# Performance work log

Hardware: AMD Instinct MI355X
Metric: run time of the kernel (lower is better)

The kernel has to match this reference:

```python
import jax, jax.numpy as jnp
import numpy as np

R = 64
N = 7

_D_PARMS = [[1], [0, 1], [8, 1, 1], [16, 25, 3, 1], [260, 153, 65, 6, 1],
            [1856, 21, 629, 137, 10, 1], [26240, 26603, 11253, 1990, 263, 15, 1]]

def _get_variance(n, r):
    res = 0.0
    for i, x in enumerate(_D_PARMS[n - 1]):
        x = float(x)
        for j in range(i):
            x *= (r - j)
        res += x
    return res

_DECAYS = [1.0] + [float(np.sqrt(_get_variance(i + 1, R) / _get_variance(i, R)))
                   for i in range(1, N)]
_DECAY_CUMSUM = float(np.sqrt(N))


def setup_inputs() -> dict:
    key = jax.random.key(0)
    M = jax.random.normal(key, (8192, R * R), dtype=jnp.float32)
    return {"M": M}


def reference(M) -> jnp.ndarray:
    shape = M.shape[:-1]
    Mm = M.reshape(shape + (R, R))            # [..., r, r]
    # power series: cumsum = sum_i (M^(i+1)) / prod(decays[:i+1]) (decays[0]=1)
    P = Mm
    acc = Mm
    for i in range(1, N):                     # fixed N=7 unrolled chain
        P = jnp.matmul(P, Mm) / _DECAYS[i]
        acc = acc + P
    # NOTE: the torch code's cumsum[..., mask, mask].zero_() operates on a copy
    # (advanced indexing), so it is a no-op on cumsum; we faithfully omit it.
    acc = acc / _DECAY_CUMSUM
    return acc.reshape(shape + (R * R,))
```

## Files before the change

### kernel.cpp

```cpp
#include <hip/hip_runtime.h>
#include <hip/hip_bf16.h>
#include <math.h>


#define RDIM 64
#define LDSP 72

using bf16x8 = __attribute__((ext_vector_type(8))) short;
using f32x4  = __attribute__((ext_vector_type(4))) float;

__device__ __forceinline__ short f2bf(float x) {
    __hip_bfloat16 h = __float2bfloat16(x);
    union { __hip_bfloat16 b; short s; } u; u.b = h; return u.s;
}
__device__ __forceinline__ float bf2f(short s) {
    union { short s; __hip_bfloat16 b; } u; u.s = s;
    return __bfloat162float(u.b);
}

__global__ __launch_bounds__(256) void power_series_kernel(
        const float* __restrict__ M, float* __restrict__ out) {
    __shared__ short PAhi[RDIM][LDSP];
    __shared__ short PAlo[RDIM][LDSP];
    __shared__ short MThi[RDIM][LDSP];
    __shared__ short MTlo[RDIM][LDSP];

    const int tid  = threadIdx.x;
    const int lane = tid & 63;
    const int wave = tid >> 6;
    const int l15  = lane & 15;
    const int quad = lane >> 4;

    const float* Mg = M   + (size_t)blockIdx.x * (RDIM * RDIM);
    float*       Og = out + (size_t)blockIdx.x * (RDIM * RDIM);

    {
        const float4* Mg4 = reinterpret_cast<const float4*>(Mg);
        #pragma unroll
        for (int v = 0; v < 4; ++v) {
            float4 x = Mg4[tid + 256 * v];
            int e0  = (tid + 256 * v) * 4;
            int row = e0 >> 6;
            int col = e0 & 63;
            float xs[4] = {x.x, x.y, x.z, x.w};
            short hs[4], ls[4];
            #pragma unroll
            for (int j = 0; j < 4; ++j) {
                short h = f2bf(xs[j]);
                hs[j] = h;
                ls[j] = f2bf(xs[j] - bf2f(h));
            }
            short4 hv; hv.x = hs[0]; hv.y = hs[1]; hv.z = hs[2]; hv.w = hs[3];
            short4 lv; lv.x = ls[0]; lv.y = ls[1]; lv.z = ls[2]; lv.w = ls[3];
            *reinterpret_cast<short4*>(&PAhi[row][col]) = hv;
            *reinterpret_cast<short4*>(&PAlo[row][col]) = lv;
            #pragma unroll
            for (int j = 0; j < 4; ++j) {
                MThi[col + j][row] = hs[j];
                MTlo[col + j][row] = ls[j];
            }
        }
    }
    __syncthreads();

    bf16x8 bhi[4][2], blo[4][2];
    #pragma unroll
    for (int t = 0; t < 4; ++t) {
        #pragma unroll
        for (int kb = 0; kb < 2; ++kb) {
            int n = t * 16 + l15;
            int k = kb * 32 + quad * 8;
            bhi[t][kb] = *reinterpret_cast<const bf16x8*>(&MThi[n][k]);
            blo[t][kb] = *reinterpret_cast<const bf16x8*>(&MTlo[n][k]);
        }
    }

    const double V[7] = {1.0, 64.0, 4104.0, 263696.0, 17021060.0,
                         1104218816.0, 72260728960.0};
    float invd[7];
    invd[0] = 1.0f;
    #pragma unroll
    for (int i = 1; i < 7; ++i) invd[i] = (float)(1.0 / sqrt(V[i] / V[i - 1]));

    f32x4 acc[4];
    #pragma unroll
    for (int t = 0; t < 4; ++t) acc[t] = (f32x4){0.f, 0.f, 0.f, 0.f};

    const int arow = wave * 16 + l15;

    #pragma unroll
    for (int s = 1; s < 7; ++s) {
        bf16x8 ahi0 = *reinterpret_cast<const bf16x8*>(&PAhi[arow][ 0 + quad * 8]);
        bf16x8 ahi1 = *reinterpret_cast<const bf16x8*>(&PAhi[arow][32 + quad * 8]);
        bf16x8 alo0 = *reinterpret_cast<const bf16x8*>(&PAlo[arow][ 0 + quad * 8]);
        bf16x8 alo1 = *reinterpret_cast<const bf16x8*>(&PAlo[arow][32 + quad * 8]);
        float inv = invd[s];
        #pragma unroll
        for (int t = 0; t < 4; ++t) {
            f32x4 c = (f32x4){0.f, 0.f, 0.f, 0.f};
            c = __builtin_amdgcn_mfma_f32_16x16x32_bf16(ahi0, bhi[t][0], c, 0, 0, 0);
            c = __builtin_amdgcn_mfma_f32_16x16x32_bf16(ahi1, bhi[t][1], c, 0, 0, 0);
            c = __builtin_amdgcn_mfma_f32_16x16x32_bf16(ahi0, blo[t][0], c, 0, 0, 0);
            c = __builtin_amdgcn_mfma_f32_16x16x32_bf16(ahi1, blo[t][1], c, 0, 0, 0);
            c = __builtin_amdgcn_mfma_f32_16x16x32_bf16(alo0, bhi[t][0], c, 0, 0, 0);
            c = __builtin_amdgcn_mfma_f32_16x16x32_bf16(alo1, bhi[t][1], c, 0, 0, 0);
            #pragma unroll
            for (int r = 0; r < 4; ++r) {
                float p = c[r] * inv;
                acc[t][r] += p;
                if (s < 6) {
                    int row = wave * 16 + quad * 4 + r;
                    int col = t * 16 + l15;
                    short h = f2bf(p);
                    PAhi[row][col] = h;
                    PAlo[row][col] = f2bf(p - bf2f(h));
                }
            }
        }
    }

    const float oscale = (float)(1.0 / sqrt(7.0));
    #pragma unroll
    for (int t = 0; t < 4; ++t) {
        #pragma unroll
        for (int r = 0; r < 4; ++r) {
            int row = wave * 16 + quad * 4 + r;
            int col = t * 16 + l15;
            float m = Mg[row * 64 + col];
            Og[row * 64 + col] = (acc[t][r] + m) * oscale;
        }
    }
}

extern "C" void kernel_launch(void* const* d_in, const int* in_sizes, int n_in,
                              void* d_out, int out_size, void* d_ws, size_t ws_size,
                              hipStream_t stream) {
    const float* M = (const float*)d_in[0];
    float* out = (float*)d_out;
    const int nmat = in_sizes[0] / (RDIM * RDIM);
    power_series_kernel<<<dim3(nmat), dim3(256), 0, stream>>>(M, out);
}
```

Baseline: 267.9 us.

## Keep power chain in registers via column-slab M·P and bpermute shuffles

Computes each power as M·P instead of P·M, so every wave owns a 16-column slab of P and keeps M's split-bf16 fragments in registers. The next step's B operand is rebuilt inside the wave with ds_bpermute shuffles rather than written to LDS and read back, which removes the per-step LDS round-trip. A single fp32 LDS copy of M is kept and reused for the final residual add instead of re-reading global memory. It also sets launch bounds to allow three blocks per CU. The cost is more register pressure and many extra cross-lane permute instructions per step.

```diff
diff --git a/kernel.cpp b/kernel.cpp
--- a/kernel.cpp
+++ b/kernel.cpp
@@ -4,32 +4,27 @@
 
 
 #define RDIM 64
-#define LDSP 72
+#define MSTR 68
 
 using bf16x8 = __attribute__((ext_vector_type(8))) short;
 using f32x4  = __attribute__((ext_vector_type(4))) float;
 
-__device__ __forceinline__ short f2bf(float x) {
-    __hip_bfloat16 h = __float2bfloat16(x);
-    union { __hip_bfloat16 b; short s; } u; u.b = h; return u.s;
+static __device__ __forceinline__ short f2bf(float x) {
+    union { __hip_bfloat16 b; short s; } u; u.b = __float2bfloat16(x); return u.s;
 }
-__device__ __forceinline__ float bf2f(short s) {
-    union { short s; __hip_bfloat16 b; } u; u.s = s;
-    return __bfloat162float(u.b);
+static __device__ __forceinline__ float bf2f(short s) {
+    union { short s2[2]; float f; } u; u.s2[0] = 0; u.s2[1] = s; return u.f;
 }
 
-__global__ __launch_bounds__(256) void power_series_kernel(
+__global__ __launch_bounds__(256, 3) void power_series_kernel(
         const float* __restrict__ M, float* __restrict__ out) {
-    __shared__ short PAhi[RDIM][LDSP];
-    __shared__ short PAlo[RDIM][LDSP];
-    __shared__ short MThi[RDIM][LDSP];
-    __shared__ short MTlo[RDIM][LDSP];
+    __shared__ float Ms[RDIM][MSTR];
 
     const int tid  = threadIdx.x;
+    const int w    = tid >> 6;
     const int lane = tid & 63;
-    const int wave = tid >> 6;
-    const int l15  = lane & 15;
-    const int quad = lane >> 4;
+    const int q    = lane >> 4;
+    const int l    = lane & 15;
 
     const float* Mg = M   + (size_t)blockIdx.x * (RDIM * RDIM);
     float*       Og = out + (size_t)blockIdx.x * (RDIM * RDIM);
@@ -38,42 +33,56 @@
         const float4* Mg4 = reinterpret_cast<const float4*>(Mg);
         #pragma unroll
         for (int v = 0; v < 4; ++v) {
-            float4 x = Mg4[tid + 256 * v];
-            int e0  = (tid + 256 * v) * 4;
-            int row = e0 >> 6;
-            int col = e0 & 63;
-            float xs[4] = {x.x, x.y, x.z, x.w};
-            short hs[4], ls[4];
-            #pragma unroll
-            for (int j = 0; j < 4; ++j) {
-                short h = f2bf(xs[j]);
-                hs[j] = h;
-                ls[j] = f2bf(xs[j] - bf2f(h));
-            }
-            short4 hv; hv.x = hs[0]; hv.y = hs[1]; hv.z = hs[2]; hv.w = hs[3];
-            short4 lv; lv.x = ls[0]; lv.y = ls[1]; lv.z = ls[2]; lv.w = ls[3];
-            *reinterpret_cast<short4*>(&PAhi[row][col]) = hv;
-            *reinterpret_cast<short4*>(&PAlo[row][col]) = lv;
-            #pragma unroll
-            for (int j = 0; j < 4; ++j) {
-                MThi[col + j][row] = hs[j];
-                MTlo[col + j][row] = ls[j];
-            }
+            int e = tid + 256 * v;
+            float4 x = Mg4[e];
+            int row = (e * 4) >> 6, col = (e * 4) & 63;
+            *reinterpret_cast<float4*>(&Ms[row][col]) = x;
         }
     }
     __syncthreads();
 
-    bf16x8 bhi[4][2], blo[4][2];
+    bf16x8 amhi[4][2], amlo[4][2];
     #pragma unroll
     for (int t = 0; t < 4; ++t) {
         #pragma unroll
         for (int kb = 0; kb < 2; ++kb) {
-            int n = t * 16 + l15;
-            int k = kb * 32 + quad * 8;
-            bhi[t][kb] = *reinterpret_cast<const bf16x8*>(&MThi[n][k]);
-            blo[t][kb] = *reinterpret_cast<const bf16x8*>(&MTlo[n][k]);
+            const float* src = &Ms[16 * t + l][32 * kb + 8 * q];
+            float4 x0 = *reinterpret_cast<const float4*>(src);
+            float4 x1 = *reinterpret_cast<const float4*>(src + 4);
+            float xs[8] = {x0.x, x0.y, x0.z, x0.w, x1.x, x1.y, x1.z, x1.w};
+            bf16x8 hv, lv;
+            #pragma unroll
+            for (int j = 0; j < 8; ++j) {
+                short h = f2bf(xs[j]); hv[j] = h;
+                lv[j] = f2bf(xs[j] - bf2f(h));
+            }
+            amhi[t][kb] = hv; amlo[t][kb] = lv;
         }
     }
+
+    bf16x8 pbhi[2], pblo[2];
+    #pragma unroll
+    for (int kb = 0; kb < 2; ++kb) {
+        float xs[8];
+        #pragma unroll
+        for (int jj = 0; jj < 8; ++jj) {
+            int j = (jj + 2 * q) & 7;
+            xs[j] = Ms[32 * kb + 8 * q + j][16 * w + l];
+        }
+        bf16x8 hv, lv;
+        #pragma unroll
+        for (int j = 0; j < 8; ++j) {
+            short h = f2bf(xs[j]); hv[j] = h;
+            lv[j] = f2bf(xs[j] - bf2f(h));
+        }
+        pbhi[kb] = hv; pblo[kb] = lv;
+    }
+
+    const int sA    = 2 * (q & 1) + (q >> 1);
+    const int addrA = ((sA << 4) + l) << 2;
+    const int addrB = ((((sA ^ 1)) << 4) + l) << 2;
+    const int qlo   = q & 1;
+    const int qhi   = q >> 1;
 
     const double V[7] = {1.0, 64.0, 4104.0, 263696.0, 17021060.0,
                          1104218816.0, 72260728960.0};
@@ -86,48 +95,74 @@
     #pragma unroll
     for (int t = 0; t < 4; ++t) acc[t] = (f32x4){0.f, 0.f, 0.f, 0.f};
 
-    const int arow = wave * 16 + l15;
-
     #pragma unroll
-    for (int s = 1; s < 7; ++s) {
-        bf16x8 ahi0 = *reinterpret_cast<const bf16x8*>(&PAhi[arow][ 0 + quad * 8]);
-        bf16x8 ahi1 = *reinterpret_cast<const bf16x8*>(&PAhi[arow][32 + quad * 8]);
-        bf16x8 alo0 = *reinterpret_cast<const bf16x8*>(&PAlo[arow][ 0 + quad * 8]);
-        bf16x8 alo1 = *reinterpret_cast<const bf16x8*>(&PAlo[arow][32 + quad * 8]);
-        float inv = invd[s];
+    for (int s = 1; s <= 6; ++s) {
+        f32x4 c[4];
         #pragma unroll
         for (int t = 0; t < 4; ++t) {
-            f32x4 c = (f32x4){0.f, 0.f, 0.f, 0.f};
-            c = __builtin_amdgcn_mfma_f32_16x16x32_bf16(ahi0, bhi[t][0], c, 0, 0, 0);
-            c = __builtin_amdgcn_mfma_f32_16x16x32_bf16(ahi1, bhi[t][1], c, 0, 0, 0);
-            c = __builtin_amdgcn_mfma_f32_16x16x32_bf16(ahi0, blo[t][0], c, 0, 0, 0);
-            c = __builtin_amdgcn_mfma_f32_16x16x32_bf16(ahi1, blo[t][1], c, 0, 0, 0);
-            c = __builtin_amdgcn_mfma_f32_16x16x32_bf16(alo0, bhi[t][0], c, 0, 0, 0);
-            c = __builtin_amdgcn_mfma_f32_16x16x32_bf16(alo1, bhi[t][1], c, 0, 0, 0);
+            f32x4 cc = (f32x4){0.f, 0.f, 0.f, 0.f};
+            cc = __builtin_amdgcn_mfma_f32_16x16x32_bf16(amhi[t][0], pbhi[0], cc, 0, 0, 0);
+            cc = __builtin_amdgcn_mfma_f32_16x16x32_bf16(amhi[t][1], pbhi[1], cc, 0, 0, 0);
+            cc = __builtin_amdgcn_mfma_f32_16x16x32_bf16(amhi[t][0], pblo[0], cc, 0, 0, 0);
+            cc = __builtin_amdgcn_mfma_f32_16x16x32_bf16(amhi[t][1], pblo[1], cc, 0, 0, 0);
+            cc = __builtin_amdgcn_mfma_f32_16x16x32_bf16(amlo[t][0], pbhi[0], cc, 0, 0, 0);
+            cc = __builtin_amdgcn_mfma_f32_16x16x32_bf16(amlo[t][1], pbhi[1], cc, 0, 0, 0);
+            c[t] = cc;
+        }
+        const float inv = invd[s];
+
+        if (s < 6) {
+            int pdh[4][2], pdl[4][2];
             #pragma unroll
-            for (int r = 0; r < 4; ++r) {
-                float p = c[r] * inv;
-                acc[t][r] += p;
-                if (s < 6) {
-                    int row = wave * 16 + quad * 4 + r;
-                    int col = t * 16 + l15;
-                    short h = f2bf(p);
-                    PAhi[row][col] = h;
-                    PAlo[row][col] = f2bf(p - bf2f(h));
+            for (int t = 0; t < 4; ++t) {
+                #pragma unroll
+                for (int h = 0; h < 2; ++h) {
+                    float a0 = c[t][2 * h] * inv, a1 = c[t][2 * h + 1] * inv;
+                    acc[t][2 * h] += a0; acc[t][2 * h + 1] += a1;
+                    short h0 = f2bf(a0), h1 = f2bf(a1);
+                    pdh[t][h] = (h0 & 0xffff) | ((int)h1 << 16);
+                    short g0 = f2bf(a0 - bf2f(h0)), g1 = f2bf(a1 - bf2f(h1));
+                    pdl[t][h] = (g0 & 0xffff) | ((int)g1 << 16);
                 }
             }
+            union { int d[4]; bf16x8 v; } nh[2], nl[2];
+            #pragma unroll
+            for (int kb = 0; kb < 2; ++kb) {
+                #pragma unroll
+                for (int h = 0; h < 2; ++h) {
+                    int zA = qlo ? pdh[2 * kb + 1][h] : pdh[2 * kb][h];
+                    int zB = qlo ? pdh[2 * kb][h]     : pdh[2 * kb + 1][h];
+                    int rA = __builtin_amdgcn_ds_bpermute(addrA, zA);
+                    int rB = __builtin_amdgcn_ds_bpermute(addrB, zB);
+                    nh[kb].d[h]     = qhi ? rB : rA;
+                    nh[kb].d[2 + h] = qhi ? rA : rB;
+                    zA = qlo ? pdl[2 * kb + 1][h] : pdl[2 * kb][h];
+                    zB = qlo ? pdl[2 * kb][h]     : pdl[2 * kb + 1][h];
+                    rA = __builtin_amdgcn_ds_bpermute(addrA, zA);
+                    rB = __builtin_amdgcn_ds_bpermute(addrB, zB);
+                    nl[kb].d[h]     = qhi ? rB : rA;
+                    nl[kb].d[2 + h] = qhi ? rA : rB;
+                }
+            }
+            pbhi[0] = nh[0].v; pbhi[1] = nh[1].v;
+            pblo[0] = nl[0].v; pblo[1] = nl[1].v;
+        } else {
+            #pragma unroll
+            for (int t = 0; t < 4; ++t)
+                #pragma unroll
+                for (int r = 0; r < 4; ++r)
+                    acc[t][r] += c[t][r] * inv;
         }
     }
 
-    const float oscale = (float)(1.0 / sqrt(7.0));
+    const float oscale = 0.3779644730092272f;
     #pragma unroll
     for (int t = 0; t < 4; ++t) {
         #pragma unroll
         for (int r = 0; r < 4; ++r) {
-            int row = wave * 16 + quad * 4 + r;
-            int col = t * 16 + l15;
-            float m = Mg[row * 64 + col];
-            Og[row * 64 + col] = (acc[t][r] + m) * oscale;
+            int row = 16 * t + 4 * q + r;
+            int col = 16 * w + l;
+            Og[row * 64 + col] = (acc[t][r] + Ms[row][col]) * oscale;
         }
     }
 }
```

After: 283.1 us. 1.06x slower.
